# Performance work log

Hardware: AMD Instinct MI355X
Metric: run time of the kernel (lower is better)

Reference implementation:

```python
import jax, jax.numpy as jnp
import numpy as np

N_NODES = 10000
N_EDGES = 640000
F_IN = 128
HID = 128
N_LAYERS = 3
N_ACT = 4096
NEG_SLOPE = 0.2


def setup_inputs() -> dict:
    key = jax.random.key(0)
    ks = jax.random.split(key, 16)
    s = 0.05
    return {
        "x": jax.random.normal(ks[0], (N_NODES, F_IN), jnp.float32),
        "edge_index": jax.random.randint(ks[1], (2, N_EDGES), 0, N_NODES, jnp.int64),
        "action_src": jax.random.randint(ks[2], (N_ACT,), 0, N_NODES, jnp.int64),
        "action_dst": jax.random.randint(ks[3], (N_ACT,), 0, N_NODES, jnp.int64),
        "action_type": jax.random.randint(ks[4], (N_ACT,), 0, 2, jnp.int32),
        "gat_W": jax.random.normal(ks[5], (N_LAYERS, HID, HID), jnp.float32) * s,
        "gat_asrc": jax.random.normal(ks[6], (N_LAYERS, HID), jnp.float32) * s,
        "gat_adst": jax.random.normal(ks[7], (N_LAYERS, HID), jnp.float32) * s,
        "gat_b": jax.random.normal(ks[8], (N_LAYERS, HID), jnp.float32) * s,
        "mlp_W1": jax.random.normal(ks[9], (2 * HID + 1, HID), jnp.float32) * s,
        "mlp_b1": jax.random.normal(ks[10], (HID,), jnp.float32) * s,
        "mlp_W2": jax.random.normal(ks[11], (HID, 1), jnp.float32) * s,
        "mlp_b2": jax.random.normal(ks[12], (1,), jnp.float32) * s,
    }


def _gat_layer(h, src, dst, W, a_src, a_dst, b, n_nodes):
    # PyG GATConv, heads=1: z = h W; e_ij = leaky_relu(a_src.z_j + a_dst.z_i)
    z = h @ W                                   # [N, HID]
    e = jax.nn.leaky_relu((z @ a_src)[src] + (z @ a_dst)[dst], NEG_SLOPE)  # [E+N]
    m = jax.ops.segment_max(e, dst, num_segments=n_nodes)
    m = jnp.where(jnp.isfinite(m), m, 0.0)
    ex = jnp.exp(e - m[dst])
    denom = jax.ops.segment_sum(ex, dst, num_segments=n_nodes)
    alpha = ex / denom[dst]                     # softmax over incoming edges
    out = jax.ops.segment_sum(alpha[:, None] * z[src], dst, num_segments=n_nodes)
    return out + b


def reference(x, edge_index, action_src, action_dst, action_type,
              gat_W, gat_asrc, gat_adst, gat_b,
              mlp_W1, mlp_b1, mlp_W2, mlp_b2):
    n = x.shape[0]
    loop = jnp.arange(n, dtype=edge_index.dtype)  # add_self_loops=True
    src = jnp.concatenate([edge_index[0], loop])
    dst = jnp.concatenate([edge_index[1], loop])
    h = x
    for l in range(N_LAYERS):
        h = jax.nn.relu(_gat_layer(h, src, dst, gat_W[l], gat_asrc[l], gat_adst[l], gat_b[l], n))
    # vectorized action scoring: [h[src], h[dst], type_flag] -> MLP -> scalar
    feat = jnp.concatenate(
        [h[action_src], h[action_dst], action_type.astype(h.dtype)[:, None]], axis=-1)
    hidden = jax.nn.relu(feat @ mlp_W1 + mlp_b1)
    scores = (hidden @ mlp_W2 + mlp_b2)[:, 0]   # [N_ACT]
    return scores
```

## Files before the change

kernel.cpp:

```cpp
#include <hip/hip_runtime.h>
#include <hip/hip_bf16.h>
#include <hip/hip_fp16.h>

#define N_NODES 10000
#define N_EDGES 640000
#define TOT_E   (N_EDGES + N_NODES)
#define HID     128
#define NEG_SLOPE 0.2f
#define N_ACT   4096

#define NBKT   250
#define NPB    40
#define P1_EPB 4096
#define P1_EPT 16
#define P1_BLOCKS 159
#define SLOTP  56
#define G_BLOCKS 313
#define AGG_B  2048

__global__ __launch_bounds__(256) void part1_k(const int* __restrict__ ei,
                                               unsigned* __restrict__ bpart,
                                               int* __restrict__ bcnt) {
    __shared__ int hist[256];
    __shared__ int lofs[256];
    __shared__ int sc[256];
    __shared__ unsigned stage[P1_EPB];
    __shared__ unsigned char bkt_of[P1_EPB];
    int t = threadIdx.x;
    hist[t] = 0;
    __syncthreads();

    unsigned pk[P1_EPT];
    int bk[P1_EPT];
    int e0 = blockIdx.x * P1_EPB;
#pragma unroll
    for (int i = 0; i < P1_EPT; i++) {
        int e = e0 + i * 256 + t;
        if (e < TOT_E) {
            int src, dst;
            if (e < N_EDGES) { src = ei[e]; dst = ei[N_EDGES + e]; }
            else             { src = e - N_EDGES; dst = src; }
            pk[i] = ((unsigned)dst << 16) | (unsigned)src;
            bk[i] = dst / NPB;
            atomicAdd(&hist[bk[i]], 1);
        } else bk[i] = -1;
    }
    __syncthreads();
    int v = hist[t];
    sc[t] = v;
    __syncthreads();
    for (int o = 1; o < 256; o <<= 1) {
        int u = (t >= o) ? sc[t - o] : 0;
        __syncthreads();
        sc[t] += u;
        __syncthreads();
    }
    lofs[t] = sc[t] - v;
    bcnt[blockIdx.x * 256 + t] = v;
    hist[t] = 0;
    __syncthreads();
#pragma unroll
    for (int i = 0; i < P1_EPT; i++) {
        if (bk[i] >= 0) {
            int p = atomicAdd(&hist[bk[i]], 1);
            int slot = lofs[bk[i]] + p;
            stage[slot] = pk[i];
            bkt_of[slot] = (unsigned char)bk[i];
        }
    }
    __syncthreads();
    int nv = min(P1_EPB, TOT_E - e0);
    for (int s = t; s < nv; s += 256) {
        int b = bkt_of[s];
        bpart[b * (P1_BLOCKS * SLOTP) + blockIdx.x * SLOTP + (s - lofs[b])] = stage[s];
    }
}

__device__ __forceinline__ void agg_node(const __half2* __restrict__ z2,
                                         const float* __restrict__ zsi, float zdn,
                                         const int* __restrict__ csr, int o0, int deg,
                                         int lane, float& accx, float& accy, float& denom) {
    for (int base = 0; base < deg; base += 64) {
        int j = base + lane;
        int sreg = 0;
        float ex = 0.f;
        if (j < deg) {
            int s = csr[o0 + j];
            sreg = s;
            float e = zsi[s] + zdn;
            e = e > 0.f ? e : NEG_SLOPE * e;
            ex = __expf(e);
        }
        int cnt = min(64, deg - base);
        int q = 0;
        for (; q + 8 <= cnt; q += 8) {
#pragma unroll
            for (int u = 0; u < 8; u++) {
                int sq = __builtin_amdgcn_readlane(sreg, q + u);
                float exq = __uint_as_float(
                    __builtin_amdgcn_readlane(__float_as_uint(ex), q + u));
                denom += exq;
                float2 vf = __half22float2(z2[sq * 64]);
                accx = fmaf(exq, vf.x, accx);
                accy = fmaf(exq, vf.y, accy);
            }
        }
        for (; q < cnt; q++) {
            int sq = __builtin_amdgcn_readlane(sreg, q);
            float exq = __uint_as_float(
                __builtin_amdgcn_readlane(__float_as_uint(ex), q));
            denom += exq;
            float2 vf = __half22float2(z2[sq * 64]);
            accx = fmaf(exq, vf.x, accx);
            accy = fmaf(exq, vf.y, accy);
        }
    }
}

__device__ __forceinline__ void gload_lds16(const float* g, float* l) {
    __builtin_amdgcn_global_load_lds(
        (const __attribute__((address_space(1))) void*)g,
        (__attribute__((address_space(3))) void*)l, 16, 0, 0);
}

__device__ __forceinline__ void gemm_body(const float* __restrict__ A,
                                          const float* __restrict__ W,
                                          const float* __restrict__ avs,
                                          const float* __restrict__ avd,
                                          __half* __restrict__ z16,
                                          float* __restrict__ zs,
                                          float* __restrict__ zd,
                                          float* smem, int blk, int t) {
    float* As = smem;
    float* Ws = smem + 32 * HID;
    int w = t >> 6, lane = t & 63;
    int row0 = blk * 32;
#pragma unroll
    for (int i = 0; i < 4; i++) {
        int chunk = w * 4 + i;
        long foff = (long)row0 * HID + chunk * 256;
        const float* g = ((foff + 256) <= (long)N_NODES * HID) ? (A + foff + lane * 4)
                                                               : (A + lane * 4);
        gload_lds16(g, As + chunk * 256);
    }
#pragma unroll
    for (int i = 0; i < 16; i++) {
        int chunk = w * 16 + i;
        gload_lds16(W + chunk * 256 + lane * 4, Ws + chunk * 256);
    }
    __syncthreads();

    int tx = t & 31, ty = t >> 5;
    int r0 = ty * 4;
    float acc[4][4] = {{0.f}};
#pragma unroll 4
    for (int k4 = 0; k4 < 32; k4++) {
        float ak[4][4];
#pragma unroll
        for (int r = 0; r < 4; r++) {
            float4 a4 = *(const float4*)&As[(r0 + r) * HID + k4 * 4];
            ak[r][0] = a4.x; ak[r][1] = a4.y; ak[r][2] = a4.z; ak[r][3] = a4.w;
        }
        const float* Wb = &Ws[k4 * 4 * HID + tx * 4];
#pragma unroll
        for (int kk = 0; kk < 4; kk++) {
            float4 wv = *(const float4*)&Wb[kk * HID];
#pragma unroll
            for (int r = 0; r < 4; r++) {
                acc[r][0] = fmaf(ak[r][kk], wv.x, acc[r][0]);
                acc[r][1] = fmaf(ak[r][kk], wv.y, acc[r][1]);
                acc[r][2] = fmaf(ak[r][kk], wv.z, acc[r][2]);
                acc[r][3] = fmaf(ak[r][kk], wv.w, acc[r][3]);
            }
        }
    }
    float4 asv = *(const float4*)&avs[tx * 4];
    float4 adv = *(const float4*)&avd[tx * 4];
#pragma unroll
    for (int r = 0; r < 4; r++) {
        int row = row0 + r0 + r;
        if (row < N_NODES) {
            *(__half2*)&z16[row * HID + tx * 4]     = __floats2half2_rn(acc[r][0], acc[r][1]);
            *(__half2*)&z16[row * HID + tx * 4 + 2] = __floats2half2_rn(acc[r][2], acc[r][3]);
        }
        float ps = acc[r][0] * asv.x + acc[r][1] * asv.y + acc[r][2] * asv.z + acc[r][3] * asv.w;
        float pd = acc[r][0] * adv.x + acc[r][1] * adv.y + acc[r][2] * adv.z + acc[r][3] * adv.w;
#pragma unroll
        for (int o = 1; o < 32; o <<= 1) {
            ps += __shfl_xor(ps, o, 64);
            pd += __shfl_xor(pd, o, 64);
        }
        if (tx == 0 && row < N_NODES) { zs[row] = ps; zd[row] = pd; }
    }
}

__global__ __launch_bounds__(256) void g2_k(const float* __restrict__ A,
                                            const float* __restrict__ W,
                                            const float* __restrict__ avs,
                                            const float* __restrict__ avd,
                                            __half* __restrict__ z16,
                                            float* __restrict__ zs,
                                            float* __restrict__ zd,
                                            const unsigned* __restrict__ bpart,
                                            const int* __restrict__ bcnt,
                                            int* __restrict__ csr,
                                            int* __restrict__ offs) {
    __shared__ float smem[20480];
    int t = threadIdx.x;

    if (blockIdx.x < G_BLOCKS) {
        gemm_body(A, W, avs, avd, z16, zs, zd, smem, blockIdx.x, t);
    } else {
        int b = blockIdx.x - G_BLOCKS;
        unsigned* ebuf = (unsigned*)smem;
        int* sc    = (int*)(smem + 4096);
        int* Ls    = sc + 256;
        int* nhist = Ls + 256;
        __shared__ int bstart_s, cnt_s;

        int tot = 0;
        if (t < NBKT) {
            int t0 = 0, t1 = 0, t2 = 0, t3 = 0;
            int blk = 0;
            for (; blk + 4 <= P1_BLOCKS; blk += 4) {
                t0 += bcnt[(blk + 0) * 256 + t];
                t1 += bcnt[(blk + 1) * 256 + t];
                t2 += bcnt[(blk + 2) * 256 + t];
                t3 += bcnt[(blk + 3) * 256 + t];
            }
            for (; blk < P1_BLOCKS; blk++) t0 += bcnt[blk * 256 + t];
            tot = t0 + t1 + t2 + t3;
        }
        sc[t] = tot;
        __syncthreads();
        for (int o = 1; o < 256; o <<= 1) {
            int u = (t >= o) ? sc[t - o] : 0;
            __syncthreads();
            sc[t] += u;
            __syncthreads();
        }
        if (t == b) { bstart_s = sc[t] - tot; cnt_s = tot; }
        if (b == 0 && t == 255) offs[N_NODES] = sc[255];
        __syncthreads();

        int L = (t < P1_BLOCKS) ? bcnt[t * 256 + b] : 0;
        Ls[t] = L;
        sc[t] = L;
        __syncthreads();
        for (int o = 1; o < 256; o <<= 1) {
            int u = (t >= o) ? sc[t - o] : 0;
            __syncthreads();
            sc[t] += u;
            __syncthreads();
        }
        if (t < NPB) nhist[t] = 0;
        {
            int wv = t >> 6, lane = t & 63;
            const unsigned* bbase = bpart + b * (P1_BLOCKS * SLOTP);
            for (int r = wv; r < P1_BLOCKS; r += 4) {
                int Lr = Ls[r];
                if (lane < Lr) ebuf[(sc[r] - Lr) + lane] = bbase[r * SLOTP + lane];
            }
        }
        __syncthreads();

        int cnt = cnt_s;
        int n0 = b * NPB;
        for (int i = t; i < cnt; i += 256) atomicAdd(&nhist[(ebuf[i] >> 16) - n0], 1);
        __syncthreads();
        if (t < 64) {
            int v2 = (t < NPB) ? nhist[t] : 0;
            int s2 = v2;
            for (int o = 1; o < 64; o <<= 1) {
                int u = __shfl_up(s2, o, 64);
                if (t >= o) s2 += u;
            }
            if (t < NPB) {
                int ofs = bstart_s + s2 - v2;
                nhist[t] = ofs;
                offs[n0 + t] = ofs;
            }
        }
        __syncthreads();
        for (int i = t; i < cnt; i += 256) {
            unsigned pk = ebuf[i];
            int p = atomicAdd(&nhist[(pk >> 16) - n0], 1);
            csr[p] = pk & 0xFFFF;
        }
    }
}

__global__ __launch_bounds__(256) void gemmh_k(const float* __restrict__ A,
                                               const float* __restrict__ W,
                                               const float* __restrict__ avs,
                                               const float* __restrict__ avd,
                                               __half* __restrict__ z16,
                                               float* __restrict__ zs,
                                               float* __restrict__ zd) {
    __shared__ float smem[20480];
    gemm_body(A, W, avs, avd, z16, zs, zd, smem, blockIdx.x, threadIdx.x);
}

__global__ __launch_bounds__(256, 8) void agg_k(const __half* __restrict__ z16,
                                                const float* __restrict__ zs,
                                                const float* __restrict__ zd,
                                                const int* __restrict__ offs,
                                                const int* __restrict__ csr,
                                                const float* __restrict__ b,
                                                float* __restrict__ hout) {
    int t = threadIdx.x;
    int w = t >> 6, lane = t & 63;
    const __half2* z2 = (const __half2*)z16 + lane;
    float2 bv = *(const float2*)&b[2 * lane];
    for (int n = blockIdx.x * 4 + w; n < N_NODES; n += AGG_B * 4) {
        int o0 = offs[n];
        int deg = offs[n + 1] - o0;
        float zdn = zd[n];
        float accx = 0.f, accy = 0.f, denom = 0.f;
        agg_node(z2, zs, zdn, csr, o0, deg, lane, accx, accy, denom);
        float inv = 1.0f / denom;
        float vx = accx * inv + bv.x;
        float vy = accy * inv + bv.y;
        float2 o;
        o.x = vx > 0.f ? vx : 0.f;
        o.y = vy > 0.f ? vy : 0.f;
        *(float2*)&hout[n * HID + 2 * lane] = o;
    }
}


#define SC_APB 16

__global__ __launch_bounds__(256) void score_k(const float* __restrict__ h,
                                               const int* __restrict__ asrc,
                                               const int* __restrict__ adst,
                                               const int* __restrict__ atype,
                                               const float* __restrict__ W1,
                                               const float* __restrict__ b1,
                                               const float* __restrict__ W2,
                                               const float* __restrict__ b2,
                                               float* __restrict__ out) {
    __shared__ float featT[257][SC_APB + 1];
    __shared__ float Wc[2][32 * HID];
    int t = threadIdx.x;
    int a0 = blockIdx.x * SC_APB;

    float4 wreg[4];
    {
        const float4* Wg = (const float4*)W1;
#pragma unroll
        for (int i = 0; i < 4; i++) wreg[i] = Wg[t + 256 * i];
    }
    for (int idx = t; idx < SC_APB * 128; idx += 256) {
        int a = idx >> 7, c = idx & 127;
        featT[c][a]       = h[asrc[a0 + a] * HID + c];
        featT[128 + c][a] = h[adst[a0 + a] * HID + c];
    }
    if (t < SC_APB) featT[256][t] = (float)atype[a0 + t];

    int cg = t & 31, ap = t >> 5;
    float4 bv = *(const float4*)&b1[cg * 4];
    float acc0[4] = {bv.x, bv.y, bv.z, bv.w};
    float acc1[4] = {bv.x, bv.y, bv.z, bv.w};

    for (int c = 0; c < 8; c++) {
        float4* dstb = (float4*)Wc[c & 1];
#pragma unroll
        for (int i = 0; i < 4; i++) dstb[t + 256 * i] = wreg[i];
        __syncthreads();
        if (c + 1 < 8) {
            const float4* Wg = (const float4*)(W1 + (c + 1) * 32 * HID);
#pragma unroll
            for (int i = 0; i < 4; i++) wreg[i] = Wg[t + 256 * i];
        }
        const float* Wb = Wc[c & 1];
        const float* fT = &featT[c * 32][0];
#pragma unroll 8
        for (int kk = 0; kk < 32; kk++) {
            float4 wv = *(const float4*)&Wb[kk * HID + cg * 4];
            float f0 = fT[kk * (SC_APB + 1) + ap * 2];
            float f1 = fT[kk * (SC_APB + 1) + ap * 2 + 1];
            acc0[0] = fmaf(f0, wv.x, acc0[0]);
            acc0[1] = fmaf(f0, wv.y, acc0[1]);
            acc0[2] = fmaf(f0, wv.z, acc0[2]);
            acc0[3] = fmaf(f0, wv.w, acc0[3]);
            acc1[0] = fmaf(f1, wv.x, acc1[0]);
            acc1[1] = fmaf(f1, wv.y, acc1[1]);
            acc1[2] = fmaf(f1, wv.z, acc1[2]);
            acc1[3] = fmaf(f1, wv.w, acc1[3]);
        }
    }
    {
        float4 wv = *(const float4*)&W1[256 * HID + cg * 4];
        float f0 = featT[256][ap * 2];
        float f1 = featT[256][ap * 2 + 1];
        acc0[0] = fmaf(f0, wv.x, acc0[0]); acc0[1] = fmaf(f0, wv.y, acc0[1]);
        acc0[2] = fmaf(f0, wv.z, acc0[2]); acc0[3] = fmaf(f0, wv.w, acc0[3]);
        acc1[0] = fmaf(f1, wv.x, acc1[0]); acc1[1] = fmaf(f1, wv.y, acc1[1]);
        acc1[2] = fmaf(f1, wv.z, acc1[2]); acc1[3] = fmaf(f1, wv.w, acc1[3]);
    }
    float4 w2v = *(const float4*)&W2[cg * 4];
    float v0 = 0.f, v1 = 0.f;
    v0 += (acc0[0] > 0.f ? acc0[0] : 0.f) * w2v.x;
    v0 += (acc0[1] > 0.f ? acc0[1] : 0.f) * w2v.y;
    v0 += (acc0[2] > 0.f ? acc0[2] : 0.f) * w2v.z;
    v0 += (acc0[3] > 0.f ? acc0[3] : 0.f) * w2v.w;
    v1 += (acc1[0] > 0.f ? acc1[0] : 0.f) * w2v.x;
    v1 += (acc1[1] > 0.f ? acc1[1] : 0.f) * w2v.y;
    v1 += (acc1[2] > 0.f ? acc1[2] : 0.f) * w2v.z;
    v1 += (acc1[3] > 0.f ? acc1[3] : 0.f) * w2v.w;
#pragma unroll
    for (int o = 1; o < 32; o <<= 1) {
        v0 += __shfl_xor(v0, o, 64);
        v1 += __shfl_xor(v1, o, 64);
    }
    if (cg == 0) {
        out[a0 + ap * 2]     = v0 + b2[0];
        out[a0 + ap * 2 + 1] = v1 + b2[0];
    }
}


extern "C" void kernel_launch(void* const* d_in, const int* in_sizes, int n_in,
                              void* d_out, int out_size, void* d_ws, size_t ws_size,
                              hipStream_t stream) {
    const float* x   = (const float*)d_in[0];
    const int* ei    = (const int*)d_in[1];
    const int* asrc  = (const int*)d_in[2];
    const int* adst  = (const int*)d_in[3];
    const int* atype = (const int*)d_in[4];
    const float* gW  = (const float*)d_in[5];
    const float* gas = (const float*)d_in[6];
    const float* gad = (const float*)d_in[7];
    const float* gb  = (const float*)d_in[8];
    const float* W1  = (const float*)d_in[9];
    const float* b1  = (const float*)d_in[10];
    const float* W2  = (const float*)d_in[11];
    const float* b2  = (const float*)d_in[12];
    float* out = (float*)d_out;

    __half* z16A = (__half*)d_ws;
    __half* z16B = z16A + N_NODES * HID;
    float* H    = (float*)(z16B + N_NODES * HID);
    float* zsA  = H + N_NODES * HID;
    float* zdA  = zsA + N_NODES;
    float* zsB  = zdA + N_NODES;
    float* zdB  = zsB + N_NODES;
    int* offs   = (int*)(zdB + N_NODES);
    int* csr    = offs + (N_NODES + 1);
    int* bcnt   = csr + TOT_E;
    unsigned* bpart = (unsigned*)(bcnt + P1_BLOCKS * 256);

    part1_k<<<P1_BLOCKS, 256, 0, stream>>>(ei, bpart, bcnt);
    g2_k<<<G_BLOCKS + NBKT, 256, 0, stream>>>(x, gW, gas, gad, z16A, zsA, zdA,
                                              bpart, bcnt, csr, offs);

    agg_k<<<AGG_B, 256, 0, stream>>>(z16A, zsA, zdA, offs, csr, gb, H);
    gemmh_k<<<G_BLOCKS, 256, 0, stream>>>(H, gW + 1 * HID * HID, gas + 1 * HID,
                                          gad + 1 * HID, z16B, zsB, zdB);
    agg_k<<<AGG_B, 256, 0, stream>>>(z16B, zsB, zdB, offs, csr, gb + 1 * HID, H);
    gemmh_k<<<G_BLOCKS, 256, 0, stream>>>(H, gW + 2 * HID * HID, gas + 2 * HID,
                                          gad + 2 * HID, z16A, zsA, zdA);
    agg_k<<<AGG_B, 256, 0, stream>>>(z16A, zsA, zdA, offs, csr, gb + 2 * HID, H);

    score_k<<<N_ACT / SC_APB, 256, 0, stream>>>(H, asrc, adst, atype,
                                                W1, b1, W2, b2, out);
}
```

Baseline: 212.4 us.

## Split each wavefront into four 16-lane groups gathering full rows with 16-byte loads

The aggregation kernel now has each 64-lane wavefront process four neighbours at once. Each 16-lane group gathers one full 256-byte fp16 row with float4 loads, instead of all 64 lanes reading 4-byte pieces of a single neighbour row. Partial sums are combined across groups with xor shuffles, and 16 lanes write the output with vector stores. The aim is fewer, wider memory instructions and more gathers in flight per wavefront. The cost is more registers, cross-lane reductions, and only 16 active lanes during the epilogue.

Measured after the change: 207.1 us. -2.5%, faster.

```diff
diff --git a/kernel.cpp b/kernel.cpp
--- a/kernel.cpp
+++ b/kernel.cpp
@@ -73,47 +73,6 @@
     for (int s = t; s < nv; s += 256) {
         int b = bkt_of[s];
         bpart[b * (P1_BLOCKS * SLOTP) + blockIdx.x * SLOTP + (s - lofs[b])] = stage[s];
-    }
-}
-
-__device__ __forceinline__ void agg_node(const __half2* __restrict__ z2,
-                                         const float* __restrict__ zsi, float zdn,
-                                         const int* __restrict__ csr, int o0, int deg,
-                                         int lane, float& accx, float& accy, float& denom) {
-    for (int base = 0; base < deg; base += 64) {
-        int j = base + lane;
-        int sreg = 0;
-        float ex = 0.f;
-        if (j < deg) {
-            int s = csr[o0 + j];
-            sreg = s;
-            float e = zsi[s] + zdn;
-            e = e > 0.f ? e : NEG_SLOPE * e;
-            ex = __expf(e);
-        }
-        int cnt = min(64, deg - base);
-        int q = 0;
-        for (; q + 8 <= cnt; q += 8) {
-#pragma unroll
-            for (int u = 0; u < 8; u++) {
-                int sq = __builtin_amdgcn_readlane(sreg, q + u);
-                float exq = __uint_as_float(
-                    __builtin_amdgcn_readlane(__float_as_uint(ex), q + u));
-                denom += exq;
-                float2 vf = __half22float2(z2[sq * 64]);
-                accx = fmaf(exq, vf.x, accx);
-                accy = fmaf(exq, vf.y, accy);
-            }
-        }
-        for (; q < cnt; q++) {
-            int sq = __builtin_amdgcn_readlane(sreg, q);
-            float exq = __uint_as_float(
-                __builtin_amdgcn_readlane(__float_as_uint(ex), q));
-            denom += exq;
-            float2 vf = __half22float2(z2[sq * 64]);
-            accx = fmaf(exq, vf.x, accx);
-            accy = fmaf(exq, vf.y, accy);
-        }
     }
 }
 
@@ -310,21 +269,65 @@
                                                 float* __restrict__ hout) {
     int t = threadIdx.x;
     int w = t >> 6, lane = t & 63;
-    const __half2* z2 = (const __half2*)z16 + lane;
-    float2 bv = *(const float2*)&b[2 * lane];
+    int grp = lane >> 4, l16 = lane & 15;
+    const char* zb = (const char*)z16;
+    unsigned loff = l16 * 16;
     for (int n = blockIdx.x * 4 + w; n < N_NODES; n += AGG_B * 4) {
         int o0 = offs[n];
         int deg = offs[n + 1] - o0;
         float zdn = zd[n];
-        float accx = 0.f, accy = 0.f, denom = 0.f;
-        agg_node(z2, zs, zdn, csr, o0, deg, lane, accx, accy, denom);
-        float inv = 1.0f / denom;
-        float vx = accx * inv + bv.x;
-        float vy = accy * inv + bv.y;
-        float2 o;
-        o.x = vx > 0.f ? vx : 0.f;
-        o.y = vy > 0.f ? vy : 0.f;
-        *(float2*)&hout[n * HID + 2 * lane] = o;
+        float acc[8] = {0.f, 0.f, 0.f, 0.f, 0.f, 0.f, 0.f, 0.f};
+        float denomv = 0.f;
+        for (int base = 0; base < deg; base += 64) {
+            int j = base + lane;
+            int sreg = 0;
+            float ex = 0.f;
+            if (j < deg) {
+                int s = csr[o0 + j];
+                sreg = s;
+                float e = zs[s] + zdn;
+                e = e > 0.f ? e : NEG_SLOPE * e;
+                ex = __expf(e);
+            }
+            int cnt = min(64, deg - base);
+            for (int q = 0; q < cnt; q += 4) {
+                int idx = q + grp;
+                int sqv = __shfl(sreg, idx, 64);
+                float exv = __shfl(ex, idx, 64);
+                float4 rv = *(const float4*)(zb + (unsigned)sqv * 256u + loff);
+                denomv += exv;
+                const __half2* hp = (const __half2*)&rv;
+#pragma unroll
+                for (int u = 0; u < 4; u++) {
+                    float2 f = __half22float2(hp[u]);
+                    acc[2 * u]     = fmaf(exv, f.x, acc[2 * u]);
+                    acc[2 * u + 1] = fmaf(exv, f.y, acc[2 * u + 1]);
+                }
+            }
+        }
+#pragma unroll
+        for (int u = 0; u < 8; u++) {
+            acc[u] += __shfl_xor(acc[u], 16, 64);
+            acc[u] += __shfl_xor(acc[u], 32, 64);
+        }
+        denomv += __shfl_xor(denomv, 16, 64);
+        denomv += __shfl_xor(denomv, 32, 64);
+        if (lane < 16) {
+            float inv = 1.0f / denomv;
+            float4 b0 = *(const float4*)&b[l16 * 8];
+            float4 b1 = *(const float4*)&b[l16 * 8 + 4];
+            float4 o0v, o1v;
+            o0v.x = fmaxf(fmaf(acc[0], inv, b0.x), 0.f);
+            o0v.y = fmaxf(fmaf(acc[1], inv, b0.y), 0.f);
+            o0v.z = fmaxf(fmaf(acc[2], inv, b0.z), 0.f);
+            o0v.w = fmaxf(fmaf(acc[3], inv, b0.w), 0.f);
+            o1v.x = fmaxf(fmaf(acc[4], inv, b1.x), 0.f);
+            o1v.y = fmaxf(fmaf(acc[5], inv, b1.y), 0.f);
+            o1v.z = fmaxf(fmaf(acc[6], inv, b1.z), 0.f);
+            o1v.w = fmaxf(fmaf(acc[7], inv, b1.w), 0.f);
+            *(float4*)&hout[(long)n * HID + l16 * 8]     = o0v;
+            *(float4*)&hout[(long)n * HID + l16 * 8 + 4] = o1v;
+        }
     }
 }
 
```
